# Kernel tuning notes

Hardware: AMD Instinct MI355X
Metric: run time of the kernel (lower is better)

## Reference

```python
import jax, jax.numpy as jnp
import numpy as np

D = 1024      # hidden_size
H = 16        # num_heads
HD = D // H   # head_dim = 64
FF = 4096     # intermediate_size
DEPTH = 2
S = 2048      # packed sequence length
NSEG = 4     # number of image segments
EPS = 1e-6


def setup_inputs() -> dict:
    key = jax.random.key(0)
    ks = jax.random.split(key, 8)
    hidden_states = jax.random.normal(ks[0], (S, D), jnp.float32)
    cu_seqlens = jnp.arange(NSEG + 1, dtype=jnp.int32) * (S // NSEG)
    # rotary embedding like RiceRotaryEmbedding(head_dim//2): freqs of dim HD//4
    # per spatial axis, h/w concatenated -> HD//2, then duplicated -> HD
    inv_freq = 1.0 / (10000.0 ** (jnp.arange(0, HD // 2, 2, dtype=jnp.float32) / (HD // 2)))
    pos = jnp.arange(S, dtype=jnp.float32)
    freqs = jnp.outer(pos, inv_freq)                       # [S, HD//4]
    emb = jnp.concatenate([freqs] * 4, axis=-1)            # [S, HD]
    cos, sin = jnp.cos(emb), jnp.sin(emb)

    def w(k, shape, fan):
        return jax.random.normal(k, shape, jnp.float32) / np.sqrt(fan)

    return {
        "hidden_states": hidden_states,
        "cu_seqlens": cu_seqlens,
        "cos": cos,
        "sin": sin,
        "ln1_g": jnp.ones((DEPTH, D), jnp.float32),
        "ln1_b": jnp.zeros((DEPTH, D), jnp.float32),
        "qkv_w": w(ks[1], (DEPTH, D, 3 * D), D),
        "qkv_b": jnp.zeros((DEPTH, 3 * D), jnp.float32),
        "proj_w": w(ks[2], (DEPTH, D, D), D),
        "proj_b": jnp.zeros((DEPTH, D), jnp.float32),
        "ln2_g": jnp.ones((DEPTH, D), jnp.float32),
        "ln2_b": jnp.zeros((DEPTH, D), jnp.float32),
        "fc1_w": w(ks[3], (DEPTH, D, FF), D),
        "fc1_b": jnp.zeros((DEPTH, FF), jnp.float32),
        "fc2_w": w(ks[4], (DEPTH, FF, D), FF),
        "fc2_b": jnp.zeros((DEPTH, D), jnp.float32),
    }


def _ln(x, g, b):
    m = jnp.mean(x, axis=-1, keepdims=True)
    v = jnp.mean(jnp.square(x - m), axis=-1, keepdims=True)
    return (x - m) / jnp.sqrt(v + EPS) * g + b


def _rotate_half(x):
    x1, x2 = jnp.split(x, 2, axis=-1)
    return jnp.concatenate([-x2, x1], axis=-1)


def reference(hidden_states, cu_seqlens, cos, sin,
              ln1_g, ln1_b, qkv_w, qkv_b, proj_w, proj_b,
              ln2_g, ln2_b, fc1_w, fc1_b, fc2_w, fc2_b):
    S_, D_ = hidden_states.shape
    # segment id per token from cu_seqlens -> block-diagonal additive mask
    seg = jnp.searchsorted(cu_seqlens[1:], jnp.arange(S_, dtype=jnp.int32), side="right")
    neg = jnp.finfo(jnp.float32).min
    bias = jnp.where(seg[:, None] == seg[None, :], 0.0, neg)   # [S, S]
    cos_e = cos[:, None, :]  # broadcast over heads, [S,1,HD]
    sin_e = sin[:, None, :]
    scale = 1.0 / np.sqrt(HD)

    x = hidden_states
    for i in range(DEPTH):
        # --- attention ---
        h = _ln(x, ln1_g[i], ln1_b[i])
        qkv = h @ qkv_w[i] + qkv_b[i]                           # [S, 3D]
        q, k, v = [t.reshape(S_, H, HD) for t in jnp.split(qkv, 3, axis=-1)]
        q = q * cos_e + _rotate_half(q) * sin_e
        k = k * cos_e + _rotate_half(k) * sin_e
        scores = jnp.einsum("shd,thd->hst", q, k) * scale + bias  # [H,S,S]
        w_ = jax.nn.softmax(scores.astype(jnp.float32), axis=-1)
        ao = jnp.einsum("hst,thd->shd", w_, v).reshape(S_, D_)
        x = x + ao @ proj_w[i] + proj_b[i]
        # --- mlp ---
        h2 = _ln(x, ln2_g[i], ln2_b[i])
        x = x + jax.nn.gelu(h2 @ fc1_w[i] + fc1_b[i], approximate=False) @ fc2_w[i] + fc2_b[i]
    return x
```

## Files before the change

kernel.cpp:

```cpp
#include <hip/hip_runtime.h>
#include <hip/hip_bf16.h>
#include <math.h>

#define Dm 1024
#define Hn 16
#define HDm 64
#define FFm 4096
#define Sn 2048
#define SEG 512
#define EPSV 1e-6f

typedef __attribute__((ext_vector_type(4))) float f32x4;
typedef __attribute__((ext_vector_type(8))) short s16x8;
typedef __attribute__((ext_vector_type(4))) short s16x4;

__device__ inline short f2bf(float f) {
  __hip_bfloat16 h = __float2bfloat16(f);
  short s;
  __builtin_memcpy(&s, &h, 2);
  return s;
}
__device__ inline float bf2f(short s) {
  unsigned u = ((unsigned)(unsigned short)s) << 16;
  float f;
  __builtin_memcpy(&f, &u, 4);
  return f;
}

__device__ inline float wred_sum(float v) {
#pragma unroll
  for (int m = 32; m > 0; m >>= 1) v += __shfl_xor(v, m, 64);
  return v;
}

__device__ inline void gld16(const short* g, short* lds_base) {
  __builtin_amdgcn_global_load_lds(
      (const __attribute__((address_space(1))) void*)g,
      (__attribute__((address_space(3))) void*)lds_base, 16, 0, 0);
}

__global__ __launch_bounds__(256) void ln_kernel(const float* __restrict__ x,
                                                 const float* __restrict__ g,
                                                 const float* __restrict__ b,
                                                 short* __restrict__ out) {
  const int row = blockIdx.x;
  const int tid = threadIdx.x;
  f32x4 v = *reinterpret_cast<const f32x4*>(x + (size_t)row * Dm + tid * 4);
  float s1 = v.x + v.y + v.z + v.w;
  float s2 = v.x * v.x + v.y * v.y + v.z * v.z + v.w * v.w;
  s1 = wred_sum(s1);
  s2 = wred_sum(s2);
  __shared__ float t1[4], t2[4];
  if ((tid & 63) == 0) { t1[tid >> 6] = s1; t2[tid >> 6] = s2; }
  __syncthreads();
  s1 = t1[0] + t1[1] + t1[2] + t1[3];
  s2 = t2[0] + t2[1] + t2[2] + t2[3];
  const float mean = s1 * (1.0f / Dm);
  const float var = s2 * (1.0f / Dm) - mean * mean;
  const float rstd = rsqrtf(var + EPSV);
  f32x4 gv = *reinterpret_cast<const f32x4*>(g + tid * 4);
  f32x4 bv = *reinterpret_cast<const f32x4*>(b + tid * 4);
  s16x4 o;
#pragma unroll
  for (int j = 0; j < 4; ++j)
    o[j] = f2bf((v[j] - mean) * rstd * gv[j] + bv[j]);
  *reinterpret_cast<s16x4*>(out + (size_t)row * Dm + tid * 4) = o;
}

template <int SPLIT>
__global__ __launch_bounds__(256) void redln_bf(const short* __restrict__ pb,
                                                const float* __restrict__ bias,
                                                const float* __restrict__ res,
                                                const float* __restrict__ g,
                                                const float* __restrict__ b,
                                                float* __restrict__ xout,
                                                short* __restrict__ h) {
  const int row = blockIdx.x;
  const int tid = threadIdx.x;
  const size_t idx = (size_t)row * Dm + tid * 4;
  f32x4 o = *reinterpret_cast<const f32x4*>(res + idx);
  o += *reinterpret_cast<const f32x4*>(bias + tid * 4);
#pragma unroll
  for (int s = 0; s < SPLIT; ++s) {
    s16x4 v = *reinterpret_cast<const s16x4*>(pb + (size_t)s * Sn * Dm + idx);
#pragma unroll
    for (int j = 0; j < 4; ++j) o[j] += bf2f(v[j]);
  }
  *reinterpret_cast<f32x4*>(xout + idx) = o;
  float s1 = o.x + o.y + o.z + o.w;
  float s2 = o.x * o.x + o.y * o.y + o.z * o.z + o.w * o.w;
  s1 = wred_sum(s1);
  s2 = wred_sum(s2);
  __shared__ float t1[4], t2[4];
  if ((tid & 63) == 0) { t1[tid >> 6] = s1; t2[tid >> 6] = s2; }
  __syncthreads();
  s1 = t1[0] + t1[1] + t1[2] + t1[3];
  s2 = t2[0] + t2[1] + t2[2] + t2[3];
  const float mean = s1 * (1.0f / Dm);
  const float var = s2 * (1.0f / Dm) - mean * mean;
  const float rstd = rsqrtf(var + EPSV);
  f32x4 gv = *reinterpret_cast<const f32x4*>(g + tid * 4);
  f32x4 bv = *reinterpret_cast<const f32x4*>(b + tid * 4);
  s16x4 ho;
#pragma unroll
  for (int j = 0; j < 4; ++j)
    ho[j] = f2bf((o[j] - mean) * rstd * gv[j] + bv[j]);
  *reinterpret_cast<s16x4*>(h + idx) = ho;
}

template <int SPLIT>
__global__ __launch_bounds__(256) void fcred_bf(const short* __restrict__ pb,
                                                const float* __restrict__ bias,
                                                const float* __restrict__ res,
                                                float* __restrict__ out) {
  const size_t i = ((size_t)blockIdx.x * 256 + threadIdx.x) * 4;
  f32x4 o = *reinterpret_cast<const f32x4*>(res + i);
  o += *reinterpret_cast<const f32x4*>(bias + (i & (Dm - 1)));
#pragma unroll
  for (int s = 0; s < SPLIT; ++s) {
    s16x4 v = *reinterpret_cast<const s16x4*>(pb + (size_t)s * Sn * Dm + i);
#pragma unroll
    for (int j = 0; j < 4; ++j) o[j] += bf2f(v[j]);
  }
  *reinterpret_cast<f32x4*>(out + i) = o;
}

struct WtJobs {
  const float* src[8];
  short* dst[8];
  int K[8], N[8], start[9];
};
__global__ __launch_bounds__(256) void wtall_kernel(WtJobs jb) {
  __shared__ float t[32][33];
  const int bid = blockIdx.x;
  int j = 0;
#pragma unroll
  for (int q = 1; q < 8; ++q)
    if (bid >= jb.start[q]) j = q;
  const int local = bid - jb.start[j];
  const int K = jb.K[j], N = jb.N[j];
  const int nx = N >> 5;
  const int n0 = (local % nx) * 32, k0 = (local / nx) * 32;
  const float* W = jb.src[j];
  short* Wt = jb.dst[j];
  const int tx = threadIdx.x & 31, ty = threadIdx.x >> 5;
#pragma unroll
  for (int r = 0; r < 32; r += 8)
    t[r + ty][tx] = W[(size_t)(k0 + r + ty) * N + n0 + tx];
  __syncthreads();
#pragma unroll
  for (int r = 0; r < 32; r += 8)
    Wt[(size_t)(n0 + r + ty) * K + k0 + tx] = f2bf(t[tx][r + ty]);
}

__global__ __launch_bounds__(256) void wtb_kernel(const short* __restrict__ V,
                                                  short* __restrict__ Vt,
                                                  int K, int N, int ldv) {
  __shared__ short t[32][34];
  const int n0 = blockIdx.x * 32, k0 = blockIdx.y * 32;
  const int tx = threadIdx.x & 31, ty = threadIdx.x >> 5;
#pragma unroll
  for (int r = 0; r < 32; r += 8)
    t[r + ty][tx] = V[(size_t)(k0 + r + ty) * ldv + n0 + tx];
  __syncthreads();
#pragma unroll
  for (int r = 0; r < 32; r += 8)
    Vt[(size_t)(n0 + r + ty) * K + k0 + tx] = t[tx][r + ty];
}

__global__ __launch_bounds__(512, 2) void qksoftpv_kernel(const short* __restrict__ qkvb,
                                                          const short* __restrict__ vT,
                                                          short* __restrict__ ao) {
  __shared__ short Ks[512 * 64];
  __shared__ short Vs[64 * 512];
  const int tid = threadIdx.x;
  const int lane = tid & 63;
  const int wave = tid >> 6;
  const int l15 = lane & 15, lg = lane >> 4, rx = l15 & 7;
  const int qblk = blockIdx.x >> 6;
  const int z = blockIdx.x & 63;
  const int seg = z & 3, head = z >> 2;

  const int srow = tid >> 3;
  const int sch = ((tid & 7) ^ (srow & 7)) * 8;

  const short* Qg = qkvb +
      (size_t)(seg * SEG + qblk * 128 + wave * 16 + l15) * 3072 + head * HDm +
      lg * 8;
  s16x8 qf0 = *reinterpret_cast<const s16x8*>(Qg);
  s16x8 qf1 = *reinterpret_cast<const s16x8*>(Qg + 32);
  __builtin_amdgcn_sched_barrier(0);
  const short* Kg = qkvb + (size_t)(seg * SEG + srow) * 3072 + Dm +
                    head * HDm + sch;
#pragma unroll
  for (int j = 0; j < 8; ++j)
    gld16(Kg + (size_t)(j * 64) * 3072, &Ks[(j * 64 + wave * 8) * 64]);
  __builtin_amdgcn_sched_barrier(0);
  {
    const short* Vg = vT + (size_t)(head * 64) * Sn + seg * SEG;
#pragma unroll
    for (int j = 0; j < 8; ++j) {
      const int d = j * 8 + wave;
      const int c = (lane & ~7) | ((lane & 7) ^ (d & 7));
      gld16(Vg + (size_t)d * Sn + c * 8, &Vs[d * 512]);
    }
  }
  asm volatile("s_waitcnt vmcnt(8)" ::: "memory");
  __builtin_amdgcn_s_barrier();
  __builtin_amdgcn_sched_barrier(0);

  f32x4 acc[32];
#pragma unroll
  for (int j = 0; j < 32; ++j) acc[j] = f32x4{0.f, 0.f, 0.f, 0.f};
  __builtin_amdgcn_s_setprio(1);
#pragma unroll
  for (int j = 0; j < 32; ++j) {
    const int R = j * 16 + l15;
    s16x8 b0 = *reinterpret_cast<const s16x8*>(&Ks[R * 64 + ((lg ^ rx) << 3)]);
    s16x8 b1 = *reinterpret_cast<const s16x8*>(
        &Ks[R * 64 + (((lg + 4) ^ rx) << 3)]);
    acc[j] = __builtin_amdgcn_mfma_f32_16x16x32_bf16(qf0, b0, acc[j], 0, 0, 0);
    acc[j] = __builtin_amdgcn_mfma_f32_16x16x32_bf16(qf1, b1, acc[j], 0, 0, 0);
  }
  __builtin_amdgcn_s_setprio(0);

  float mx[4], inv[4];
#pragma unroll
  for (int r = 0; r < 4; ++r) {
    float m = acc[0][r];
#pragma unroll
    for (int j = 1; j < 32; ++j) m = fmaxf(m, acc[j][r]);
#pragma unroll
    for (int d = 1; d < 16; d <<= 1) m = fmaxf(m, __shfl_xor(m, d, 64));
    mx[r] = m * 0.125f;
  }
#pragma unroll
  for (int r = 0; r < 4; ++r) {
    float s = 0.f;
#pragma unroll
    for (int j = 0; j < 32; ++j) {
      float pv = __expf(acc[j][r] * 0.125f - mx[r]);
      acc[j][r] = pv;
      s += pv;
    }
#pragma unroll
    for (int d = 1; d < 16; d <<= 1) s += __shfl_xor(s, d, 64);
    inv[r] = 1.0f / s;
  }

  __syncthreads();
  asm volatile("s_waitcnt vmcnt(0)" ::: "memory");

  short* Ps = Ks;
  f32x4 pv[4] = {};
  const int q2 = wave * 16 + l15;
  const int sxr = (q2 ^ (q2 >> 3)) & 7;
#pragma unroll
  for (int kh = 0; kh < 2; ++kh) {
#pragma unroll
    for (int jj = 0; jj < 16; ++jj) {
      const int j = kh * 16 + jj;
#pragma unroll
      for (int r = 0; r < 4; ++r) {
        const int q = wave * 16 + lg * 4 + r;
        const int kp = jj * 16 + l15;
        const int c = kp >> 3;
        const int sxw = (q ^ (q >> 3)) & 7;
        const int cs = (c & 24) | ((c & 7) ^ sxw);
        Ps[q * 256 + cs * 8 + (kp & 7)] = f2bf(acc[j][r]);
      }
    }
    asm volatile("s_waitcnt lgkmcnt(0)" ::: "memory");
    __builtin_amdgcn_sched_barrier(0);
    __builtin_amdgcn_s_setprio(1);
#pragma unroll
    for (int ks = 0; ks < 8; ++ks) {
      const int ca = ks * 4 + lg;
      const int csa = (ca & 24) | ((ca & 7) ^ sxr);
      s16x8 pa = *reinterpret_cast<const s16x8*>(&Ps[q2 * 256 + csa * 8]);
#pragma unroll
      for (int fj = 0; fj < 4; ++fj) {
        const int d = fj * 16 + l15;
        const int cb = kh * 32 + ks * 4 + lg;
        const int csb = (cb & ~7) | ((cb & 7) ^ (d & 7));
        s16x8 pb = *reinterpret_cast<const s16x8*>(&Vs[d * 512 + csb * 8]);
        pv[fj] = __builtin_amdgcn_mfma_f32_16x16x32_bf16(pa, pb, pv[fj], 0, 0, 0);
      }
    }
    __builtin_amdgcn_s_setprio(0);
    asm volatile("s_waitcnt lgkmcnt(0)" ::: "memory");
    __builtin_amdgcn_sched_barrier(0);
  }

#pragma unroll
  for (int r = 0; r < 4; ++r) {
    const float iv = inv[r];
    const size_t rowg =
        (size_t)(seg * SEG + qblk * 128 + wave * 16 + lg * 4 + r) * Dm +
        head * 64;
#pragma unroll
    for (int fj = 0; fj < 4; ++fj)
      ao[rowg + fj * 16 + l15] = f2bf(pv[fj][r] * iv);
  }
}

struct GemmArgs {
  const short* A; int lda;
  const short* B; int ldb;
  void* C; int ldc;
  int M, N, K;
  const float* bias;
  const float* cosb; const float* sinb;
  float scale;
};

template <int BM, int BN, int SPLIT, int MODE>
__global__ __launch_bounds__(256) void gemm6(GemmArgs p) {
  constexpr int WN = 2;
  constexpr int WM = 2;
  constexpr int FI = BM / WM / 16;
  constexpr int FJ = BN / WN / 16;
  const int z = blockIdx.z;
  const short* A = p.A;
  const short* B = p.B;
  char* Cb = (char*)p.C;
  int kbase = 0, nkt = p.K >> 6;
  const int gx = gridDim.x;
  const int nwg = gx * gridDim.y;
  const int orig = blockIdx.y * gx + blockIdx.x;
  const int sid = (orig & 7) * (nwg >> 3) + (orig >> 3);
  const int tileM = (sid / gx) * BM;
  const int tileN = (sid % gx) * BN;
  if (MODE == 6) {
    kbase = z * (p.K / SPLIT);
    nkt = (p.K / SPLIT) >> 6;
    Cb += (size_t)z * p.M * p.N * 2;
  }
  __shared__ short As[BM * 64];
  __shared__ short Bs[BN * 64];
  const int tid = threadIdx.x;
  const int lane = tid & 63;
  const int wave = tid >> 6;
  const int l15 = lane & 15;
  const int lg = lane >> 4;
  const int rx = l15 & 7;
  const int wr = (wave / WN) * (BM / WM);
  const int wc = (wave % WN) * (BN / WN);
  const int srow = lane >> 3;
  const int scol = ((lane & 7) ^ srow) * 8;

  f32x4 acc[FI][FJ] = {};

  const short* Ag = A + (size_t)(tileM + wave * 8 + srow) * p.lda + scol + kbase;
  const short* Bg = B + (size_t)(tileN + wave * 8 + srow) * p.ldb + scol + kbase;

  for (int kt = 0; kt < nkt; ++kt) {
    const int k0 = kt * 64;
#pragma unroll
    for (int j = 0; j < BM / 32; ++j)
      gld16(Ag + (size_t)(j * 32) * p.lda + k0, &As[(j * 32 + wave * 8) * 64]);
#pragma unroll
    for (int j = 0; j < BN / 32; ++j)
      gld16(Bg + (size_t)(j * 32) * p.ldb + k0, &Bs[(j * 32 + wave * 8) * 64]);
    __syncthreads();
#pragma unroll
    for (int kk = 0; kk < 64; kk += 32) {
      const int kkc = kk >> 3;
      s16x8 af[FI], bfr[FJ];
#pragma unroll
      for (int f = 0; f < FI; ++f)
        af[f] = *reinterpret_cast<const s16x8*>(
            &As[(wr + f * 16 + l15) * 64 + (((lg + kkc) ^ rx) << 3)]);
#pragma unroll
      for (int f = 0; f < FJ; ++f)
        bfr[f] = *reinterpret_cast<const s16x8*>(
            &Bs[(wc + f * 16 + l15) * 64 + (((lg + kkc) ^ rx) << 3)]);
#pragma unroll
      for (int fi = 0; fi < FI; ++fi)
#pragma unroll
        for (int fj = 0; fj < FJ; ++fj)
          acc[fi][fj] = __builtin_amdgcn_mfma_f32_16x16x32_bf16(
              af[fi], bfr[fj], acc[fi][fj], 0, 0, 0);
    }
    __syncthreads();
  }

  if (MODE == 4) {
    short* Cs = (short*)Cb;
    const bool isqk = (tileN + wc) < 2048;
#pragma unroll
    for (int fi = 0; fi < FI; ++fi) {
#pragma unroll
      for (int fj = 0; fj < FJ; ++fj) {
#pragma unroll
        for (int r = 0; r < 4; ++r) {
          const int row = tileM + wr + fi * 16 + lg * 4 + r;
          const int col = tileN + wc + fj * 16 + l15;
          float a0 = acc[fi][fj][r] + p.bias[col];
          float vout;
          if (isqk) {
            float a1 = acc[fi][fj ^ 2][r] + p.bias[col ^ 32];
            const int dl = fj * 16 + l15;
            const float c = p.cosb[(size_t)row * HDm + dl];
            const float sn = p.sinb[(size_t)row * HDm + dl];
            vout = (fj < 2) ? (a0 * c - a1 * sn) : (a0 * c + a1 * sn);
          } else {
            vout = a0;
          }
          Cs[(size_t)row * p.ldc + col] = f2bf(vout);
        }
      }
    }
    return;
  }

#pragma unroll
  for (int fi = 0; fi < FI; ++fi) {
#pragma unroll
    for (int fj = 0; fj < FJ; ++fj) {
#pragma unroll
      for (int r = 0; r < 4; ++r) {
        const int row = tileM + wr + fi * 16 + lg * 4 + r;
        const int col = tileN + wc + fj * 16 + l15;
        float v = acc[fi][fj][r];
        if (MODE == 5) {
          v += p.bias[col];
          v = 0.5f * v * (1.0f + erff(v * 0.70710678118654752f));
        }
        reinterpret_cast<short*>(Cb)[(size_t)row * p.ldc + col] = f2bf(v);
      }
    }
  }
}

extern "C" void kernel_launch(void* const* d_in, const int* in_sizes, int n_in,
                              void* d_out, int out_size, void* d_ws, size_t ws_size,
                              hipStream_t stream) {
  const float* x0 = (const float*)d_in[0];
  const float* cosb = (const float*)d_in[2];
  const float* sinb = (const float*)d_in[3];
  const float* ln1_g = (const float*)d_in[4];
  const float* ln1_b = (const float*)d_in[5];
  const float* qkv_w = (const float*)d_in[6];
  const float* qkv_b = (const float*)d_in[7];
  const float* proj_w = (const float*)d_in[8];
  const float* proj_b = (const float*)d_in[9];
  const float* ln2_g = (const float*)d_in[10];
  const float* ln2_b = (const float*)d_in[11];
  const float* fc1_w = (const float*)d_in[12];
  const float* fc1_b = (const float*)d_in[13];
  const float* fc2_w = (const float*)d_in[14];
  const float* fc2_b = (const float*)d_in[15];

  char* ws = (char*)d_ws;
  size_t off = 0;
  auto alloc = [&](size_t bytes) {
    void* p = ws + off;
    off += (bytes + 255) & ~(size_t)255;
    return p;
  };
  short* wqkvT = (short*)alloc((size_t)2 * 3072 * 1024 * 2);
  short* wprojT = (short*)alloc((size_t)2 * 1024 * 1024 * 2);
  short* wfc1T = (short*)alloc((size_t)2 * 4096 * 1024 * 2);
  short* wfc2T = (short*)alloc((size_t)2 * 1024 * 4096 * 2);
  float* xbuf = (float*)alloc((size_t)Sn * Dm * 4);
  short* hbuf = (short*)alloc((size_t)Sn * Dm * 2);
  short* qkvb = (short*)alloc((size_t)Sn * 3 * Dm * 2);
  float* pbuf = (float*)alloc((size_t)4 * Sn * Dm * 4);
  short* pbufS = (short*)pbuf;
  short* ao = (short*)alloc((size_t)Sn * Dm * 2);
  short* ffn = (short*)alloc((size_t)Sn * FFm * 2);
  short* vT = ffn;
  (void)ws_size; (void)in_sizes; (void)n_in; (void)out_size;

  {
    WtJobs jb;
    int acc = 0;
    for (int i = 0; i < 2; ++i) {
      const int base = i * 4;
      jb.src[base + 0] = qkv_w + (size_t)i * Dm * 3072;
      jb.dst[base + 0] = wqkvT + (size_t)i * 3072 * Dm;
      jb.K[base + 0] = Dm; jb.N[base + 0] = 3072;
      jb.src[base + 1] = proj_w + (size_t)i * Dm * Dm;
      jb.dst[base + 1] = wprojT + (size_t)i * Dm * Dm;
      jb.K[base + 1] = Dm; jb.N[base + 1] = Dm;
      jb.src[base + 2] = fc1_w + (size_t)i * Dm * FFm;
      jb.dst[base + 2] = wfc1T + (size_t)i * FFm * Dm;
      jb.K[base + 2] = Dm; jb.N[base + 2] = FFm;
      jb.src[base + 3] = fc2_w + (size_t)i * FFm * Dm;
      jb.dst[base + 3] = wfc2T + (size_t)i * Dm * FFm;
      jb.K[base + 3] = FFm; jb.N[base + 3] = Dm;
    }
    for (int j = 0; j < 8; ++j) {
      jb.start[j] = acc;
      acc += (jb.N[j] >> 5) * (jb.K[j] >> 5);
    }
    jb.start[8] = acc;
    wtall_kernel<<<dim3(acc), 256, 0, stream>>>(jb);
  }

  ln_kernel<<<dim3(Sn), 256, 0, stream>>>(x0, ln1_g, ln1_b, hbuf);

  for (int i = 0; i < 2; ++i) {
    const float* xin = i ? (const float*)xbuf : x0;

    {
      GemmArgs p = {};
      p.A = hbuf; p.lda = Dm;
      p.B = wqkvT + (size_t)i * 3072 * Dm; p.ldb = Dm;
      p.C = qkvb; p.ldc = 3 * Dm;
      p.M = Sn; p.N = 3 * Dm; p.K = Dm;
      p.bias = qkv_b + i * 3 * Dm; p.cosb = cosb; p.sinb = sinb;
      gemm6<64, 128, 1, 4><<<dim3(24, 32, 1), 256, 0, stream>>>(p);
    }

    wtb_kernel<<<dim3(32, 64), 256, 0, stream>>>(qkvb + 2 * Dm, vT, Sn, Dm, 3 * Dm);

    qksoftpv_kernel<<<dim3(256), 512, 0, stream>>>(qkvb, vT, ao);

    {
      GemmArgs p = {};
      p.A = ao; p.lda = Dm;
      p.B = wprojT + (size_t)i * Dm * Dm; p.ldb = Dm;
      p.C = pbufS; p.ldc = Dm;
      p.M = Sn; p.N = Dm; p.K = Dm;
      gemm6<64, 64, 2, 6><<<dim3(16, 32, 2), 256, 0, stream>>>(p);
    }
    redln_bf<2><<<dim3(Sn), 256, 0, stream>>>(
        pbufS, proj_b + i * Dm, xin, ln2_g + i * Dm, ln2_b + i * Dm, xbuf, hbuf);

    {
      GemmArgs p = {};
      p.A = hbuf; p.lda = Dm;
      p.B = wfc1T + (size_t)i * FFm * Dm; p.ldb = Dm;
      p.C = ffn; p.ldc = FFm;
      p.M = Sn; p.N = FFm; p.K = Dm;
      p.bias = fc1_b + i * FFm;
      gemm6<64, 128, 1, 5><<<dim3(32, 32, 1), 256, 0, stream>>>(p);
    }

    {
      GemmArgs p = {};
      p.A = ffn; p.lda = FFm;
      p.B = wfc2T + (size_t)i * Dm * FFm; p.ldb = FFm;
      p.C = pbufS; p.ldc = Dm;
      p.M = Sn; p.N = Dm; p.K = FFm;
      gemm6<64, 128, 4, 6><<<dim3(8, 32, 4), 256, 0, stream>>>(p);
    }
    if (i == 0) {
      redln_bf<4><<<dim3(Sn), 256, 0, stream>>>(
          pbufS, fc2_b, xbuf, ln1_g + Dm, ln1_b + Dm, xbuf, hbuf);
    } else {
      fcred_bf<4><<<dim3(Sn * Dm / 1024), 256, 0, stream>>>(
          pbufS, fc2_b + Dm, xbuf, (float*)d_out);
    }
  }
}
```

Baseline: 272.3 us.

## Restructure attention: 64-query blocks, blocked V layout read directly from global

The V transpose now writes a 32-key-blocked layout, so the attention kernel reads V fragments straight from global/L2 instead of staging them in LDS. The attention kernel moves to 256-thread blocks of 64 queries, doubling the grid, and each wave keeps its own P tile in the freed LDS, so the PV product runs in a single pass. This aims to cut LDS use and raise occupancy, at the cost of uncoalesced global V loads issued inside the MFMA loop and K being reloaded by twice as many blocks.

Result: slower. 278.3 us (+2.2%).

```diff
diff --git a/kernel.cpp b/kernel.cpp
--- a/kernel.cpp
+++ b/kernel.cpp
@@ -153,26 +153,26 @@
     Wt[(size_t)(n0 + r + ty) * K + k0 + tx] = f2bf(t[tx][r + ty]);
 }
 
-__global__ __launch_bounds__(256) void wtb_kernel(const short* __restrict__ V,
-                                                  short* __restrict__ Vt,
-                                                  int K, int N, int ldv) {
+__global__ __launch_bounds__(256) void wtb2_kernel(const short* __restrict__ V,
+                                                   short* __restrict__ Vt2,
+                                                   int ldv) {
   __shared__ short t[32][34];
-  const int n0 = blockIdx.x * 32, k0 = blockIdx.y * 32;
+  const int n0 = blockIdx.x * 32;
+  const int kb = blockIdx.y;
   const int tx = threadIdx.x & 31, ty = threadIdx.x >> 5;
 #pragma unroll
   for (int r = 0; r < 32; r += 8)
-    t[r + ty][tx] = V[(size_t)(k0 + r + ty) * ldv + n0 + tx];
+    t[r + ty][tx] = V[(size_t)(kb * 32 + r + ty) * ldv + n0 + tx];
   __syncthreads();
 #pragma unroll
   for (int r = 0; r < 32; r += 8)
-    Vt[(size_t)(n0 + r + ty) * K + k0 + tx] = t[tx][r + ty];
-}
-
-__global__ __launch_bounds__(512, 2) void qksoftpv_kernel(const short* __restrict__ qkvb,
-                                                          const short* __restrict__ vT,
-                                                          short* __restrict__ ao) {
+    Vt2[((size_t)kb * 1024 + n0 + r + ty) * 32 + tx] = t[tx][r + ty];
+}
+
+__global__ __launch_bounds__(256, 2) void attn3_kernel(const short* __restrict__ qkvb,
+                                                       const short* __restrict__ vT2,
+                                                       short* __restrict__ ao) {
   __shared__ short Ks[512 * 64];
-  __shared__ short Vs[64 * 512];
   const int tid = threadIdx.x;
   const int lane = tid & 63;
   const int wave = tid >> 6;
@@ -180,32 +180,20 @@
   const int qblk = blockIdx.x >> 6;
   const int z = blockIdx.x & 63;
   const int seg = z & 3, head = z >> 2;
-
-  const int srow = tid >> 3;
-  const int sch = ((tid & 7) ^ (srow & 7)) * 8;
-
-  const short* Qg = qkvb +
-      (size_t)(seg * SEG + qblk * 128 + wave * 16 + l15) * 3072 + head * HDm +
-      lg * 8;
+  const int qbase = seg * SEG + qblk * 64 + wave * 16;
+
+  const short* Qg = qkvb + (size_t)(qbase + l15) * 3072 + head * HDm + lg * 8;
   s16x8 qf0 = *reinterpret_cast<const s16x8*>(Qg);
   s16x8 qf1 = *reinterpret_cast<const s16x8*>(Qg + 32);
   __builtin_amdgcn_sched_barrier(0);
+  const int srow = tid >> 3;
+  const int sch = ((tid & 7) ^ (srow & 7)) * 8;
   const short* Kg = qkvb + (size_t)(seg * SEG + srow) * 3072 + Dm +
                     head * HDm + sch;
 #pragma unroll
-  for (int j = 0; j < 8; ++j)
-    gld16(Kg + (size_t)(j * 64) * 3072, &Ks[(j * 64 + wave * 8) * 64]);
-  __builtin_amdgcn_sched_barrier(0);
-  {
-    const short* Vg = vT + (size_t)(head * 64) * Sn + seg * SEG;
-#pragma unroll
-    for (int j = 0; j < 8; ++j) {
-      const int d = j * 8 + wave;
-      const int c = (lane & ~7) | ((lane & 7) ^ (d & 7));
-      gld16(Vg + (size_t)d * Sn + c * 8, &Vs[d * 512]);
-    }
-  }
-  asm volatile("s_waitcnt vmcnt(8)" ::: "memory");
+  for (int j = 0; j < 16; ++j)
+    gld16(Kg + (size_t)(j * 32) * 3072, &Ks[(j * 32 + wave * 8) * 64]);
+  asm volatile("s_waitcnt vmcnt(0)" ::: "memory");
   __builtin_amdgcn_s_barrier();
   __builtin_amdgcn_sched_barrier(0);
 
@@ -249,55 +237,45 @@
   }
 
   __syncthreads();
-  asm volatile("s_waitcnt vmcnt(0)" ::: "memory");
-
-  short* Ps = Ks;
+
+  short* Pw = Ks + wave * 16 * 512;
+#pragma unroll
+  for (int j = 0; j < 32; ++j) {
+#pragma unroll
+    for (int r = 0; r < 4; ++r) {
+      const int q = lg * 4 + r;
+      const int kp = j * 16 + l15;
+      const int c = kp >> 3;
+      const int sxw = (q ^ (q >> 3)) & 7;
+      const int cs = (c & ~7) | ((c & 7) ^ sxw);
+      Pw[q * 512 + cs * 8 + (kp & 7)] = f2bf(acc[j][r]);
+    }
+  }
+  asm volatile("s_waitcnt lgkmcnt(0)" ::: "memory");
+  __builtin_amdgcn_sched_barrier(0);
+
   f32x4 pv[4] = {};
-  const int q2 = wave * 16 + l15;
-  const int sxr = (q2 ^ (q2 >> 3)) & 7;
-#pragma unroll
-  for (int kh = 0; kh < 2; ++kh) {
-#pragma unroll
-    for (int jj = 0; jj < 16; ++jj) {
-      const int j = kh * 16 + jj;
-#pragma unroll
-      for (int r = 0; r < 4; ++r) {
-        const int q = wave * 16 + lg * 4 + r;
-        const int kp = jj * 16 + l15;
-        const int c = kp >> 3;
-        const int sxw = (q ^ (q >> 3)) & 7;
-        const int cs = (c & 24) | ((c & 7) ^ sxw);
-        Ps[q * 256 + cs * 8 + (kp & 7)] = f2bf(acc[j][r]);
-      }
-    }
-    asm volatile("s_waitcnt lgkmcnt(0)" ::: "memory");
-    __builtin_amdgcn_sched_barrier(0);
-    __builtin_amdgcn_s_setprio(1);
-#pragma unroll
-    for (int ks = 0; ks < 8; ++ks) {
-      const int ca = ks * 4 + lg;
-      const int csa = (ca & 24) | ((ca & 7) ^ sxr);
-      s16x8 pa = *reinterpret_cast<const s16x8*>(&Ps[q2 * 256 + csa * 8]);
-#pragma unroll
-      for (int fj = 0; fj < 4; ++fj) {
-        const int d = fj * 16 + l15;
-        const int cb = kh * 32 + ks * 4 + lg;
-        const int csb = (cb & ~7) | ((cb & 7) ^ (d & 7));
-        s16x8 pb = *reinterpret_cast<const s16x8*>(&Vs[d * 512 + csb * 8]);
-        pv[fj] = __builtin_amdgcn_mfma_f32_16x16x32_bf16(pa, pb, pv[fj], 0, 0, 0);
-      }
-    }
-    __builtin_amdgcn_s_setprio(0);
-    asm volatile("s_waitcnt lgkmcnt(0)" ::: "memory");
-    __builtin_amdgcn_sched_barrier(0);
-  }
+  const int sxr = (l15 ^ (l15 >> 3)) & 7;
+  const short* Vg = vT2 + ((size_t)(seg * 16) * 1024 + head * HDm) * 32;
+  __builtin_amdgcn_s_setprio(1);
+#pragma unroll
+  for (int ks = 0; ks < 16; ++ks) {
+    const int ca = ks * 4 + lg;
+    const int csa = (ca & ~7) | ((ca & 7) ^ sxr);
+    s16x8 pa = *reinterpret_cast<const s16x8*>(&Pw[l15 * 512 + csa * 8]);
+#pragma unroll
+    for (int fj = 0; fj < 4; ++fj) {
+      s16x8 pb = *reinterpret_cast<const s16x8*>(
+          Vg + ((size_t)ks * 1024 + fj * 16 + l15) * 32 + lg * 8);
+      pv[fj] = __builtin_amdgcn_mfma_f32_16x16x32_bf16(pa, pb, pv[fj], 0, 0, 0);
+    }
+  }
+  __builtin_amdgcn_s_setprio(0);
 
 #pragma unroll
   for (int r = 0; r < 4; ++r) {
     const float iv = inv[r];
-    const size_t rowg =
-        (size_t)(seg * SEG + qblk * 128 + wave * 16 + lg * 4 + r) * Dm +
-        head * 64;
+    const size_t rowg = (size_t)(qbase + lg * 4 + r) * Dm + head * 64;
 #pragma unroll
     for (int fj = 0; fj < 4; ++fj)
       ao[rowg + fj * 16 + l15] = f2bf(pv[fj][r] * iv);
@@ -470,7 +448,7 @@
   short* pbufS = (short*)pbuf;
   short* ao = (short*)alloc((size_t)Sn * Dm * 2);
   short* ffn = (short*)alloc((size_t)Sn * FFm * 2);
-  short* vT = ffn;
+  short* vT2 = ffn;
   (void)ws_size; (void)in_sizes; (void)n_in; (void)out_size;
 
   {
@@ -514,9 +492,9 @@
       gemm6<64, 128, 1, 4><<<dim3(24, 32, 1), 256, 0, stream>>>(p);
     }
 
-    wtb_kernel<<<dim3(32, 64), 256, 0, stream>>>(qkvb + 2 * Dm, vT, Sn, Dm, 3 * Dm);
-
-    qksoftpv_kernel<<<dim3(256), 512, 0, stream>>>(qkvb, vT, ao);
+    wtb2_kernel<<<dim3(32, 64), 256, 0, stream>>>(qkvb + 2 * Dm, vT2, 3 * Dm);
+
+    attn3_kernel<<<dim3(512), 256, 0, stream>>>(qkvb, vT2, ao);
 
     {
       GemmArgs p = {};
```
